# Optimization experiments

Measured on AMD Instinct MI355X. Metric: run time of the kernel, lower is better.

Reference implementation:

```python
import jax, jax.numpy as jnp
import numpy as np

SCORER_BIAS = 0.0
LN_EPS = 1e-5


def setup_inputs() -> dict:
    key = jax.random.key(0)
    k0, k1, k2 = jax.random.split(key, 3)
    B, L, D, H = 8, 8192, 1024, 256
    features = jax.random.normal(k0, (B, L, D), dtype=jnp.float32)
    gamma = jnp.ones((D,), jnp.float32)
    beta = jnp.zeros((D,), jnp.float32)
    W1 = (jax.random.normal(k1, (D, H)) * (1.0 / np.sqrt(D))).astype(jnp.float32)
    b1 = jnp.zeros((H,), jnp.float32)
    W2 = (jax.random.normal(k2, (H, 1)) * (1.0 / np.sqrt(H))).astype(jnp.float32)
    b2 = jnp.zeros((1,), jnp.float32)
    return {"features": features, "gamma": gamma, "beta": beta,
            "W1": W1, "b1": b1, "W2": W2, "b2": b2, "k": 512}


def reference(features, gamma, beta, W1, b1, W2, b2, k):
    # LayerNorm over last dim D
    mu = jnp.mean(features, axis=-1, keepdims=True)
    var = jnp.mean(jnp.square(features - mu), axis=-1, keepdims=True)
    x = (features - mu) * jax.lax.rsqrt(var + LN_EPS) * gamma + beta  # [B,L,D]
    # small MLP scorer: Linear -> GELU(exact, matches torch default) -> Linear
    h = jax.nn.gelu(jnp.einsum('bld,dh->blh', x, W1) + b1, approximate=False)
    scores = (jnp.einsum('blh,ho->blo', h, W2) + b2)[..., 0] + SCORER_BIAS  # [B,L]
    # per-row top-k (torch.topk semantics: largest, sorted)
    _, idx = jax.lax.top_k(scores, k)  # [B,k] int32
    # batched gather of original (un-normalized) features
    selected = jnp.take_along_axis(features, idx[..., None], axis=1)  # [B,k,D]
    return selected, scores, idx
```

## Files before the change

### kernel.cpp

```cpp
#include <hip/hip_runtime.h>
#include <math.h>

#define Dk 1024
#define Hk 256
#define Lk 8192
#define Bk 8
#define MTOT (Bk*Lk)

typedef _Float16 f16;
typedef __attribute__((ext_vector_type(8))) _Float16 f16x8;
typedef __attribute__((ext_vector_type(4))) float f32x4;
typedef unsigned long long u64;

#define AKG 520
#define ASP (8*AKG)
#define ABUF (2*ASP)

__global__ __launch_bounds__(1024) void prep_split(
    const float* __restrict__ W1, const float* __restrict__ gamma,
    const float* __restrict__ beta, f16* __restrict__ W1F,
    float* __restrict__ Spart, float* __restrict__ Tpart) {
  __shared__ float ps[1024], pt[1024];
  const int b = blockIdx.x, t = threadIdx.x;
  float sa = 0.f, ta = 0.f;
  #pragma unroll
  for (int j = 0; j < 4; ++j) {
    int idx = j * 65536 + b * 1024 + t;
    int d = idx >> 8, h = idx & 255;
    float w = W1[idx];
    float g = gamma[d];
    sa = fmaf(g, w, sa);
    ta = fmaf(beta[d], w, ta);
    float wg = g * w;
    f16 whi = (f16)wg;
    f16 wlp = (f16)((wg - (float)whi) * 2048.f);
    int ks = d >> 6, kg = (d >> 3) & 7, kk = d & 7;
    int nf = h >> 4, nn = h & 15;
    size_t base = ((((size_t)ks * 2) * 16 + nf) * 8 + kg) * 128 + nn * 8 + kk;
    W1F[base] = whi;
    W1F[base + 16384] = wlp;
  }
  ps[t] = sa; pt[t] = ta;
  __syncthreads();
  if (t < 256) {
    Spart[b * 256 + t] = ps[t] + ps[t + 256] + ps[t + 512] + ps[t + 768];
    Tpart[b * 256 + t] = pt[t] + pt[t + 256] + pt[t + 512] + pt[t + 768];
  }
}

__global__ __launch_bounds__(256) void prep_combine(
    const float* __restrict__ Spart, const float* __restrict__ Tpart,
    const float* __restrict__ b1, float* __restrict__ S, float* __restrict__ Tb) {
  int j = threadIdx.x;
  float s = 0.f, t = 0.f;
  for (int b = 0; b < 64; ++b) { s += Spart[b * 256 + j]; t += Tpart[b * 256 + j]; }
  S[j] = s;
  Tb[j] = t + b1[j];
}

#define MM3(aA, aB, ah, ax, wh, wl)                                            \
  aA = __builtin_amdgcn_mfma_f32_16x16x32_f16(ah, wh, aA, 0, 0, 0);            \
  aB = __builtin_amdgcn_mfma_f32_16x16x32_f16(ah, wl, aB, 0, 0, 0);            \
  aB = __builtin_amdgcn_mfma_f32_16x16x32_f16(ax, wh, aB, 0, 0, 0);

__global__ __launch_bounds__(512, 4) void scores_mfma(
    const float* __restrict__ F, const f16* __restrict__ W1F,
    const float* __restrict__ S, const float* __restrict__ Tb,
    const float* __restrict__ W2, const float* __restrict__ b2,
    float* __restrict__ scores_out) {
  __shared__ f16 As[2][ABUF];
  __shared__ float smu[64], srs[64];
  __shared__ float sred[64][4];

  const int tid = threadIdx.x;
  const int RM = blockIdx.x * 64;
  const int wid = tid >> 6, lane = tid & 63;
  const int wm = wid & 1, wn = wid >> 1;
  const int lg = lane >> 4, l15 = lane & 15;

  const int arow = tid >> 3, kg = tid & 7;
  const float* Aptr = F + (size_t)(RM + arow) * Dk + kg * 8;

  const int aoff0 = lg * AKG + (wm * 32 + l15) * 8;
  const int bwoff = (wn * 4) * 1024 + lg * 128 + l15 * 8;

  f32x4 accA[2][4], accB[2][4];
  #pragma unroll
  for (int i = 0; i < 2; ++i)
    #pragma unroll
    for (int j = 0; j < 4; ++j) {
      accA[i][j] = (f32x4){0.f, 0.f, 0.f, 0.f};
      accB[i][j] = (f32x4){0.f, 0.f, 0.f, 0.f};
    }

  float rsum = 0.f, rsq = 0.f;

#define SPLIT_STORE(buf, av0, av1)                                             \
  {                                                                            \
    f16x8 vhi, vlo;                                                            \
    _Pragma("unroll")                                                          \
    for (int e = 0; e < 8; ++e) {                                              \
      float x = (e < 4) ? ((e == 0) ? av0.x : (e == 1) ? av0.y                 \
                           : (e == 2) ? av0.z : av0.w)                         \
                        : ((e == 4) ? av1.x : (e == 5) ? av1.y                 \
                           : (e == 6) ? av1.z : av1.w);                        \
      rsum += x; rsq = fmaf(x, x, rsq);                                        \
      f16 hi = (f16)x;                                                         \
      vhi[e] = hi;                                                             \
      vlo[e] = (f16)((x - (float)hi) * 2048.f);                                \
    }                                                                          \
    *reinterpret_cast<f16x8*>(&As[buf][kg * AKG + arow * 8]) = vhi;            \
    *reinterpret_cast<f16x8*>(&As[buf][ASP + kg * AKG + arow * 8]) = vlo;      \
  }

  float4 av0 = *reinterpret_cast<const float4*>(Aptr);
  float4 av1 = *reinterpret_cast<const float4*>(Aptr + 4);
  SPLIT_STORE(0, av0, av1)
  av0 = *reinterpret_cast<const float4*>(Aptr + 64);
  av1 = *reinterpret_cast<const float4*>(Aptr + 68);
  __syncthreads();

  for (int s = 0; s < 16; ++s) {
    const int cur = s & 1;
    const f16* bs = W1F + (size_t)s * 32768 + bwoff;

    {
      f16x8 wh0 = *reinterpret_cast<const f16x8*>(bs);
      f16x8 wh1 = *reinterpret_cast<const f16x8*>(bs + 1024);
      f16x8 wl0 = *reinterpret_cast<const f16x8*>(bs + 16384);
      f16x8 wl1 = *reinterpret_cast<const f16x8*>(bs + 17408);
      const f16* ab = &As[cur][aoff0];
      f16x8 ahi0 = *reinterpret_cast<const f16x8*>(ab);
      f16x8 ahi1 = *reinterpret_cast<const f16x8*>(ab + 128);
      f16x8 axl0 = *reinterpret_cast<const f16x8*>(ab + ASP);
      f16x8 axl1 = *reinterpret_cast<const f16x8*>(ab + ASP + 128);
      if (s < 15) {
        SPLIT_STORE(cur ^ 1, av0, av1)
        if (s < 14) {
          av0 = *reinterpret_cast<const float4*>(Aptr + (s + 2) * 64);
          av1 = *reinterpret_cast<const float4*>(Aptr + (s + 2) * 64 + 4);
        }
      }
      MM3(accA[0][0], accB[0][0], ahi0, axl0, wh0, wl0)
      MM3(accA[1][0], accB[1][0], ahi1, axl1, wh0, wl0)
      MM3(accA[0][1], accB[0][1], ahi0, axl0, wh1, wl1)
      MM3(accA[1][1], accB[1][1], ahi1, axl1, wh1, wl1)
      wh0 = *reinterpret_cast<const f16x8*>(bs + 2048);
      wh1 = *reinterpret_cast<const f16x8*>(bs + 3072);
      wl0 = *reinterpret_cast<const f16x8*>(bs + 2048 + 16384);
      wl1 = *reinterpret_cast<const f16x8*>(bs + 3072 + 16384);
      MM3(accA[0][2], accB[0][2], ahi0, axl0, wh0, wl0)
      MM3(accA[1][2], accB[1][2], ahi1, axl1, wh0, wl0)
      MM3(accA[0][3], accB[0][3], ahi0, axl0, wh1, wl1)
      MM3(accA[1][3], accB[1][3], ahi1, axl1, wh1, wl1)
    }
    {
      f16x8 wh0 = *reinterpret_cast<const f16x8*>(bs + 512);
      f16x8 wh1 = *reinterpret_cast<const f16x8*>(bs + 512 + 1024);
      f16x8 wl0 = *reinterpret_cast<const f16x8*>(bs + 512 + 16384);
      f16x8 wl1 = *reinterpret_cast<const f16x8*>(bs + 512 + 17408);
      const f16* ab = &As[cur][aoff0 + 4 * AKG];
      f16x8 ahi0 = *reinterpret_cast<const f16x8*>(ab);
      f16x8 ahi1 = *reinterpret_cast<const f16x8*>(ab + 128);
      f16x8 axl0 = *reinterpret_cast<const f16x8*>(ab + ASP);
      f16x8 axl1 = *reinterpret_cast<const f16x8*>(ab + ASP + 128);
      MM3(accA[0][0], accB[0][0], ahi0, axl0, wh0, wl0)
      MM3(accA[1][0], accB[1][0], ahi1, axl1, wh0, wl0)
      MM3(accA[0][1], accB[0][1], ahi0, axl0, wh1, wl1)
      MM3(accA[1][1], accB[1][1], ahi1, axl1, wh1, wl1)
      wh0 = *reinterpret_cast<const f16x8*>(bs + 512 + 2048);
      wh1 = *reinterpret_cast<const f16x8*>(bs + 512 + 3072);
      wl0 = *reinterpret_cast<const f16x8*>(bs + 512 + 2048 + 16384);
      wl1 = *reinterpret_cast<const f16x8*>(bs + 512 + 3072 + 16384);
      MM3(accA[0][2], accB[0][2], ahi0, axl0, wh0, wl0)
      MM3(accA[1][2], accB[1][2], ahi1, axl1, wh0, wl0)
      MM3(accA[0][3], accB[0][3], ahi0, axl0, wh1, wl1)
      MM3(accA[1][3], accB[1][3], ahi1, axl1, wh1, wl1)
    }
    __syncthreads();
  }

  rsum += __shfl_xor(rsum, 1); rsum += __shfl_xor(rsum, 2); rsum += __shfl_xor(rsum, 4);
  rsq  += __shfl_xor(rsq, 1);  rsq  += __shfl_xor(rsq, 2);  rsq  += __shfl_xor(rsq, 4);
  if ((tid & 7) == 0) {
    float mu  = rsum * (1.f / 1024.f);
    float var = rsq * (1.f / 1024.f) - mu * mu;
    smu[arow] = mu;
    srs[arow] = rsqrtf(var + 1e-5f);
  }
  __syncthreads();

  float s2[4], tb2[4], w2v[4];
  #pragma unroll
  for (int nf = 0; nf < 4; ++nf) {
    int col = (wn * 4 + nf) * 16 + l15;
    s2[nf] = S[col]; tb2[nf] = Tb[col]; w2v[nf] = W2[col];
  }
  #pragma unroll
  for (int mf = 0; mf < 2; ++mf) {
    const int rbase = wm * 32 + mf * 16 + lg * 4;
    #pragma unroll
    for (int reg = 0; reg < 4; ++reg) {
      const int row = rbase + reg;
      float mu = smu[row], rs = srs[row];
      float part = 0.f;
      #pragma unroll
      for (int nf = 0; nf < 4; ++nf) {
        float val = accA[mf][nf][reg] + accB[mf][nf][reg] * (1.f / 2048.f);
        float hpre = rs * val - rs * mu * s2[nf] + tb2[nf];
        float g = 0.5f * hpre * (1.f + erff(hpre * 0.70710678118654752f));
        part = fmaf(g, w2v[nf], part);
      }
      part += __shfl_xor(part, 1); part += __shfl_xor(part, 2);
      part += __shfl_xor(part, 4); part += __shfl_xor(part, 8);
      if (l15 == 0) sred[row][wn] = part;
    }
  }
  __syncthreads();
  if (tid < 64) {
    float sc = b2[0] + sred[tid][0] + sred[tid][1] + sred[tid][2] + sred[tid][3];
    scores_out[RM + tid] = sc;
  }
}

__global__ __launch_bounds__(512) void topk_stage1(
    const float* __restrict__ scores, u64* __restrict__ kout) {
  __shared__ u64 keys[1024];
  const int blk = blockIdx.x;
  const int batch = blk >> 3, chunk = blk & 7;
  const int t = threadIdx.x;
  #pragma unroll
  for (int j = 0; j < 2; ++j) {
    int i = t + j * 512;
    int gi = chunk * 1024 + i;
    unsigned u = __float_as_uint(scores[(size_t)batch * Lk + gi]);
    unsigned mono = (u & 0x80000000u) ? ~u : (u | 0x80000000u);
    keys[i] = ((u64)(~mono) << 32) | (unsigned)gi;
  }
  __syncthreads();
  for (int size = 2; size <= 1024; size <<= 1) {
    for (int stride = size >> 1; stride > 0; stride >>= 1) {
      int lo = ((t & ~(stride - 1)) << 1) | (t & (stride - 1));
      int hi = lo + stride;
      bool up = ((lo & size) == 0);
      u64 a = keys[lo], c = keys[hi];
      if ((a > c) == up) { keys[lo] = c; keys[hi] = a; }
      __syncthreads();
    }
  }
  kout[(size_t)blk * 512 + t] = keys[t];
}

__global__ __launch_bounds__(512) void topk_stage2(
    const u64* __restrict__ kin, int k,
    float* __restrict__ idx_f, int* __restrict__ idx_i) {
  __shared__ u64 kk[4096];
  __shared__ u64 tmp[2048];
  const int b = blockIdx.x, t = threadIdx.x;
  #pragma unroll
  for (int j = 0; j < 8; ++j) kk[t + j * 512] = kin[(size_t)b * 4096 + t + j * 512];
  __syncthreads();
  #pragma unroll
  for (int j = 0; j < 4; ++j) {
    u64 a = kk[j * 1024 + t];
    u64 c = kk[j * 1024 + 512 + (511 - t)];
    tmp[j * 512 + t] = a < c ? a : c;
  }
  __syncthreads();
  for (int stride = 256; stride > 0; stride >>= 1) {
    #pragma unroll
    for (int w = 0; w < 2; ++w) {
      int p = t + w * 512;
      int r = p >> 8, q = p & 255;
      int lo = r * 512 + (((q & ~(stride - 1)) << 1) | (q & (stride - 1)));
      u64 a = tmp[lo], c = tmp[lo + stride];
      if (a > c) { tmp[lo] = c; tmp[lo + stride] = a; }
    }
    __syncthreads();
  }
  #pragma unroll
  for (int j = 0; j < 2; ++j) {
    u64 a = tmp[j * 1024 + t];
    u64 c = tmp[j * 1024 + 512 + (511 - t)];
    kk[j * 512 + t] = a < c ? a : c;
  }
  __syncthreads();
  for (int stride = 256; stride > 0; stride >>= 1) {
    int r = t >> 8, q = t & 255;
    int lo = r * 512 + (((q & ~(stride - 1)) << 1) | (q & (stride - 1)));
    u64 a = kk[lo], c = kk[lo + stride];
    if (a > c) { kk[lo] = c; kk[lo + stride] = a; }
    __syncthreads();
  }
  {
    u64 a = kk[t];
    u64 c = kk[512 + (511 - t)];
    tmp[t] = a < c ? a : c;
  }
  __syncthreads();
  for (int stride = 256; stride > 0; stride >>= 1) {
    if (t < 256) {
      int lo = ((t & ~(stride - 1)) << 1) | (t & (stride - 1));
      u64 a = tmp[lo], c = tmp[lo + stride];
      if (a > c) { tmp[lo] = c; tmp[lo + stride] = a; }
    }
    __syncthreads();
  }
  if (t < k) {
    int id = (int)(tmp[t] & 0xFFFFFFFFu);
    idx_f[(size_t)b * k + t] = (float)id;
    idx_i[(size_t)b * k + t] = id;
  }
}

__global__ __launch_bounds__(256) void gather_kernel(
    const float* __restrict__ F, const int* __restrict__ idx,
    float* __restrict__ out, int k) {
  int row = blockIdx.x;
  int b = row / k;
  int id = idx[row];
  const float4* src = reinterpret_cast<const float4*>(F + ((size_t)b * Lk + id) * Dk);
  float4* dst = reinterpret_cast<float4*>(out + (size_t)row * Dk);
  dst[threadIdx.x] = src[threadIdx.x];
}

extern "C" void kernel_launch(void* const* d_in, const int* in_sizes, int n_in,
                              void* d_out, int out_size, void* d_ws, size_t ws_size,
                              hipStream_t stream) {
  const float* F     = (const float*)d_in[0];
  const float* gamma = (const float*)d_in[1];
  const float* beta  = (const float*)d_in[2];
  const float* W1    = (const float*)d_in[3];
  const float* b1    = (const float*)d_in[4];
  const float* W2    = (const float*)d_in[5];
  const float* b2    = (const float*)d_in[6];
  int k = (out_size - Bk * Lk) / (Bk * Dk + Bk);

  float* out_sel = (float*)d_out;
  float* out_sc  = out_sel + (size_t)Bk * k * Dk;
  float* out_idx = out_sc + (size_t)Bk * Lk;

  f16*   W1F   = (f16*)d_ws;
  u64*   kout  = (u64*)((char*)d_ws + (1 << 20));
  float* Spart = (float*)((char*)kout + 262144);
  float* Tpart = Spart + 16384;
  float* Sp    = Tpart + 16384;
  float* Tbp   = Sp + Hk;
  int*   idxi  = (int*)(Tbp + Hk);

  hipLaunchKernelGGL(prep_split,   dim3(64),        dim3(1024), 0, stream,
                     W1, gamma, beta, W1F, Spart, Tpart);
  hipLaunchKernelGGL(prep_combine, dim3(1),         dim3(Hk),   0, stream,
                     Spart, Tpart, b1, Sp, Tbp);
  hipLaunchKernelGGL(scores_mfma,  dim3(MTOT / 64), dim3(512),  0, stream,
                     F, W1F, Sp, Tbp, W2, b2, out_sc);
  hipLaunchKernelGGL(topk_stage1,  dim3(64),        dim3(512),  0, stream,
                     out_sc, kout);
  hipLaunchKernelGGL(topk_stage2,  dim3(Bk),        dim3(512),  0, stream,
                     kout, k, out_idx, idxi);
  hipLaunchKernelGGL(gather_kernel, dim3(Bk * k),   dim3(256),  0, stream,
                     F, idxi, out_sel, k);
}
```

Measured before the change: 161.8 us.

## Stage W1 tiles in LDS via direct global-to-LDS loads with larger row tiles

The scores kernel now uses 128-row tiles with 1024 threads and a K step of 32 instead of 64. Each K step's split fp16 W1 tile is loaded once per block into double-buffered shared memory with global_load_lds, so warps no longer each read W1 from global or L2. W1F is repacked to match the new layout. The aim is to cut redundant weight traffic and improve reuse, at the cost of more barriers (32 steps), more LDS per block, and possibly lower occupancy.

```diff
diff --git a/kernel.cpp b/kernel.cpp
--- a/kernel.cpp
+++ b/kernel.cpp
@@ -9,12 +9,19 @@
 
 typedef _Float16 f16;
 typedef __attribute__((ext_vector_type(8))) _Float16 f16x8;
+typedef __attribute__((ext_vector_type(4))) _Float16 f16x4;
 typedef __attribute__((ext_vector_type(4))) float f32x4;
 typedef unsigned long long u64;
 
-#define AKG 520
-#define ASP (8*AKG)
+#define AROW 40
+#define ASP (128*AROW)
 #define ABUF (2*ASP)
+#define BSTEP 16384
+
+#define GLD_LDS16(g, l)                                                        \
+  __builtin_amdgcn_global_load_lds(                                            \
+      (const __attribute__((address_space(1))) unsigned int*)(g),              \
+      (__attribute__((address_space(3))) unsigned int*)(l), 16, 0, 0)
 
 __global__ __launch_bounds__(1024) void prep_split(
     const float* __restrict__ W1, const float* __restrict__ gamma,
@@ -34,11 +41,11 @@
     float wg = g * w;
     f16 whi = (f16)wg;
     f16 wlp = (f16)((wg - (float)whi) * 2048.f);
-    int ks = d >> 6, kg = (d >> 3) & 7, kk = d & 7;
+    int ks = d >> 5, kg = (d >> 3) & 3, kk = d & 7;
     int nf = h >> 4, nn = h & 15;
-    size_t base = ((((size_t)ks * 2) * 16 + nf) * 8 + kg) * 128 + nn * 8 + kk;
+    size_t base = (size_t)ks * BSTEP + (size_t)nf * 512 + kg * 128 + nn * 8 + kk;
     W1F[base] = whi;
-    W1F[base + 16384] = wlp;
+    W1F[base + 8192] = wlp;
   }
   ps[t] = sa; pt[t] = ta;
   __syncthreads();
@@ -63,119 +70,86 @@
   aB = __builtin_amdgcn_mfma_f32_16x16x32_f16(ah, wl, aB, 0, 0, 0);            \
   aB = __builtin_amdgcn_mfma_f32_16x16x32_f16(ax, wh, aB, 0, 0, 0);
 
-__global__ __launch_bounds__(512, 4) void scores_mfma(
+__global__ __launch_bounds__(1024) void scores_mfma(
     const float* __restrict__ F, const f16* __restrict__ W1F,
     const float* __restrict__ S, const float* __restrict__ Tb,
     const float* __restrict__ W2, const float* __restrict__ b2,
     float* __restrict__ scores_out) {
-  __shared__ f16 As[2][ABUF];
-  __shared__ float smu[64], srs[64];
-  __shared__ float sred[64][4];
+  __shared__ __align__(16) f16 As[2][ABUF];
+  __shared__ __align__(16) f16 Bs[2][BSTEP];
+  __shared__ float smu[128], srs[128];
+  __shared__ float sred[128][8];
 
   const int tid = threadIdx.x;
-  const int RM = blockIdx.x * 64;
+  const int RM = blockIdx.x * 128;
   const int wid = tid >> 6, lane = tid & 63;
   const int wm = wid & 1, wn = wid >> 1;
   const int lg = lane >> 4, l15 = lane & 15;
 
-  const int arow = tid >> 3, kg = tid & 7;
-  const float* Aptr = F + (size_t)(RM + arow) * Dk + kg * 8;
-
-  const int aoff0 = lg * AKG + (wm * 32 + l15) * 8;
-  const int bwoff = (wn * 4) * 1024 + lg * 128 + l15 * 8;
-
-  f32x4 accA[2][4], accB[2][4];
-  #pragma unroll
-  for (int i = 0; i < 2; ++i)
-    #pragma unroll
-    for (int j = 0; j < 4; ++j) {
+  const int arow = tid >> 3, sub = tid & 7;
+  const int awoff = arow * AROW + (sub >> 1) * 8 + (sub & 1) * 4;
+  const float* Aptr = F + (size_t)(RM + arow) * Dk + sub * 4;
+
+  const int aoff = (wm * 64 + l15) * AROW + lg * 8;
+  const int boff = (wn * 2) * 512 + lg * 128 + l15 * 8;
+
+  f32x4 accA[4][2], accB[4][2];
+  #pragma unroll
+  for (int i = 0; i < 4; ++i)
+    #pragma unroll
+    for (int j = 0; j < 2; ++j) {
       accA[i][j] = (f32x4){0.f, 0.f, 0.f, 0.f};
       accB[i][j] = (f32x4){0.f, 0.f, 0.f, 0.f};
     }
 
   float rsum = 0.f, rsq = 0.f;
 
-#define SPLIT_STORE(buf, av0, av1)                                             \
+#define SPLIT4(buf, fv)                                                        \
   {                                                                            \
-    f16x8 vhi, vlo;                                                            \
+    f16x4 vhi, vlo;                                                            \
     _Pragma("unroll")                                                          \
-    for (int e = 0; e < 8; ++e) {                                              \
-      float x = (e < 4) ? ((e == 0) ? av0.x : (e == 1) ? av0.y                 \
-                           : (e == 2) ? av0.z : av0.w)                         \
-                        : ((e == 4) ? av1.x : (e == 5) ? av1.y                 \
-                           : (e == 6) ? av1.z : av1.w);                        \
+    for (int e = 0; e < 4; ++e) {                                              \
+      float x = (e == 0) ? fv.x : (e == 1) ? fv.y : (e == 2) ? fv.z : fv.w;    \
       rsum += x; rsq = fmaf(x, x, rsq);                                        \
       f16 hi = (f16)x;                                                         \
       vhi[e] = hi;                                                             \
       vlo[e] = (f16)((x - (float)hi) * 2048.f);                                \
     }                                                                          \
-    *reinterpret_cast<f16x8*>(&As[buf][kg * AKG + arow * 8]) = vhi;            \
-    *reinterpret_cast<f16x8*>(&As[buf][ASP + kg * AKG + arow * 8]) = vlo;      \
-  }
-
-  float4 av0 = *reinterpret_cast<const float4*>(Aptr);
-  float4 av1 = *reinterpret_cast<const float4*>(Aptr + 4);
-  SPLIT_STORE(0, av0, av1)
-  av0 = *reinterpret_cast<const float4*>(Aptr + 64);
-  av1 = *reinterpret_cast<const float4*>(Aptr + 68);
-  __syncthreads();
-
-  for (int s = 0; s < 16; ++s) {
+    *reinterpret_cast<f16x4*>(&As[buf][awoff])       = vhi;                    \
+    *reinterpret_cast<f16x4*>(&As[buf][ASP + awoff]) = vlo;                    \
+  }
+
+#define STAGE_B(buf, step)                                                     \
+  {                                                                            \
+    const f16* bsrc = W1F + (size_t)(step) * BSTEP;                            \
+    GLD_LDS16(bsrc + (size_t)tid * 8, &Bs[buf][tid * 8]);                      \
+    GLD_LDS16(bsrc + (size_t)(1024 + tid) * 8, &Bs[buf][(1024 + tid) * 8]);    \
+  }
+
+  STAGE_B(0, 0)
+  float4 av = *reinterpret_cast<const float4*>(Aptr);
+  SPLIT4(0, av)
+  av = *reinterpret_cast<const float4*>(Aptr + 32);
+  __syncthreads();
+
+  for (int s = 0; s < 32; ++s) {
     const int cur = s & 1;
-    const f16* bs = W1F + (size_t)s * 32768 + bwoff;
-
-    {
-      f16x8 wh0 = *reinterpret_cast<const f16x8*>(bs);
-      f16x8 wh1 = *reinterpret_cast<const f16x8*>(bs + 1024);
-      f16x8 wl0 = *reinterpret_cast<const f16x8*>(bs + 16384);
-      f16x8 wl1 = *reinterpret_cast<const f16x8*>(bs + 17408);
-      const f16* ab = &As[cur][aoff0];
-      f16x8 ahi0 = *reinterpret_cast<const f16x8*>(ab);
-      f16x8 ahi1 = *reinterpret_cast<const f16x8*>(ab + 128);
-      f16x8 axl0 = *reinterpret_cast<const f16x8*>(ab + ASP);
-      f16x8 axl1 = *reinterpret_cast<const f16x8*>(ab + ASP + 128);
-      if (s < 15) {
-        SPLIT_STORE(cur ^ 1, av0, av1)
-        if (s < 14) {
-          av0 = *reinterpret_cast<const float4*>(Aptr + (s + 2) * 64);
-          av1 = *reinterpret_cast<const float4*>(Aptr + (s + 2) * 64 + 4);
-        }
-      }
-      MM3(accA[0][0], accB[0][0], ahi0, axl0, wh0, wl0)
-      MM3(accA[1][0], accB[1][0], ahi1, axl1, wh0, wl0)
-      MM3(accA[0][1], accB[0][1], ahi0, axl0, wh1, wl1)
-      MM3(accA[1][1], accB[1][1], ahi1, axl1, wh1, wl1)
-      wh0 = *reinterpret_cast<const f16x8*>(bs + 2048);
-      wh1 = *reinterpret_cast<const f16x8*>(bs + 3072);
-      wl0 = *reinterpret_cast<const f16x8*>(bs + 2048 + 16384);
-      wl1 = *reinterpret_cast<const f16x8*>(bs + 3072 + 16384);
-      MM3(accA[0][2], accB[0][2], ahi0, axl0, wh0, wl0)
-      MM3(accA[1][2], accB[1][2], ahi1, axl1, wh0, wl0)
-      MM3(accA[0][3], accB[0][3], ahi0, axl0, wh1, wl1)
-      MM3(accA[1][3], accB[1][3], ahi1, axl1, wh1, wl1)
-    }
-    {
-      f16x8 wh0 = *reinterpret_cast<const f16x8*>(bs + 512);
-      f16x8 wh1 = *reinterpret_cast<const f16x8*>(bs + 512 + 1024);
-      f16x8 wl0 = *reinterpret_cast<const f16x8*>(bs + 512 + 16384);
-      f16x8 wl1 = *reinterpret_cast<const f16x8*>(bs + 512 + 17408);
-      const f16* ab = &As[cur][aoff0 + 4 * AKG];
-      f16x8 ahi0 = *reinterpret_cast<const f16x8*>(ab);
-      f16x8 ahi1 = *reinterpret_cast<const f16x8*>(ab + 128);
-      f16x8 axl0 = *reinterpret_cast<const f16x8*>(ab + ASP);
-      f16x8 axl1 = *reinterpret_cast<const f16x8*>(ab + ASP + 128);
-      MM3(accA[0][0], accB[0][0], ahi0, axl0, wh0, wl0)
-      MM3(accA[1][0], accB[1][0], ahi1, axl1, wh0, wl0)
-      MM3(accA[0][1], accB[0][1], ahi0, axl0, wh1, wl1)
-      MM3(accA[1][1], accB[1][1], ahi1, axl1, wh1, wl1)
-      wh0 = *reinterpret_cast<const f16x8*>(bs + 512 + 2048);
-      wh1 = *reinterpret_cast<const f16x8*>(bs + 512 + 3072);
-      wl0 = *reinterpret_cast<const f16x8*>(bs + 512 + 2048 + 16384);
-      wl1 = *reinterpret_cast<const f16x8*>(bs + 512 + 3072 + 16384);
-      MM3(accA[0][2], accB[0][2], ahi0, axl0, wh0, wl0)
-      MM3(accA[1][2], accB[1][2], ahi1, axl1, wh0, wl0)
-      MM3(accA[0][3], accB[0][3], ahi0, axl0, wh1, wl1)
-      MM3(accA[1][3], accB[1][3], ahi1, axl1, wh1, wl1)
+    if (s < 31) {
+      STAGE_B(cur ^ 1, s + 1)
+      SPLIT4(cur ^ 1, av)
+      if (s < 30) av = *reinterpret_cast<const float4*>(Aptr + (s + 2) * 32);
+    }
+    f16x8 wh0 = *reinterpret_cast<const f16x8*>(&Bs[cur][boff]);
+    f16x8 wl0 = *reinterpret_cast<const f16x8*>(&Bs[cur][boff + 8192]);
+    f16x8 wh1 = *reinterpret_cast<const f16x8*>(&Bs[cur][boff + 512]);
+    f16x8 wl1 = *reinterpret_cast<const f16x8*>(&Bs[cur][boff + 512 + 8192]);
+    #pragma unroll
+    for (int mf = 0; mf < 4; ++mf) {
+      const int ao = aoff + mf * (16 * AROW);
+      f16x8 ahi = *reinterpret_cast<const f16x8*>(&As[cur][ao]);
+      f16x8 axl = *reinterpret_cast<const f16x8*>(&As[cur][ASP + ao]);
+      MM3(accA[mf][0], accB[mf][0], ahi, axl, wh0, wl0)
+      MM3(accA[mf][1], accB[mf][1], ahi, axl, wh1, wl1)
     }
     __syncthreads();
   }
@@ -190,22 +164,22 @@
   }
   __syncthreads();
 
-  float s2[4], tb2[4], w2v[4];
-  #pragma unroll
-  for (int nf = 0; nf < 4; ++nf) {
-    int col = (wn * 4 + nf) * 16 + l15;
+  float s2[2], tb2[2], w2v[2];
+  #pragma unroll
+  for (int nf = 0; nf < 2; ++nf) {
+    int col = wn * 32 + nf * 16 + l15;
     s2[nf] = S[col]; tb2[nf] = Tb[col]; w2v[nf] = W2[col];
   }
   #pragma unroll
-  for (int mf = 0; mf < 2; ++mf) {
-    const int rbase = wm * 32 + mf * 16 + lg * 4;
+  for (int mf = 0; mf < 4; ++mf) {
+    const int rbase = wm * 64 + mf * 16 + lg * 4;
     #pragma unroll
     for (int reg = 0; reg < 4; ++reg) {
       const int row = rbase + reg;
       float mu = smu[row], rs = srs[row];
       float part = 0.f;
       #pragma unroll
-      for (int nf = 0; nf < 4; ++nf) {
+      for (int nf = 0; nf < 2; ++nf) {
         float val = accA[mf][nf][reg] + accB[mf][nf][reg] * (1.f / 2048.f);
         float hpre = rs * val - rs * mu * s2[nf] + tb2[nf];
         float g = 0.5f * hpre * (1.f + erff(hpre * 0.70710678118654752f));
@@ -217,8 +191,10 @@
     }
   }
   __syncthreads();
-  if (tid < 64) {
-    float sc = b2[0] + sred[tid][0] + sred[tid][1] + sred[tid][2] + sred[tid][3];
+  if (tid < 128) {
+    float sc = b2[0];
+    #pragma unroll
+    for (int w = 0; w < 8; ++w) sc += sred[tid][w];
     scores_out[RM + tid] = sc;
   }
 }
@@ -348,16 +324,16 @@
   float* Tbp   = Sp + Hk;
   int*   idxi  = (int*)(Tbp + Hk);
 
-  hipLaunchKernelGGL(prep_split,   dim3(64),        dim3(1024), 0, stream,
+  hipLaunchKernelGGL(prep_split,   dim3(64),         dim3(1024), 0, stream,
                      W1, gamma, beta, W1F, Spart, Tpart);
-  hipLaunchKernelGGL(prep_combine, dim3(1),         dim3(Hk),   0, stream,
+  hipLaunchKernelGGL(prep_combine, dim3(1),          dim3(Hk),   0, stream,
                      Spart, Tpart, b1, Sp, Tbp);
-  hipLaunchKernelGGL(scores_mfma,  dim3(MTOT / 64), dim3(512),  0, stream,
+  hipLaunchKernelGGL(scores_mfma,  dim3(MTOT / 128), dim3(1024), 0, stream,
                      F, W1F, Sp, Tbp, W2, b2, out_sc);
-  hipLaunchKernelGGL(topk_stage1,  dim3(64),        dim3(512),  0, stream,
+  hipLaunchKernelGGL(topk_stage1,  dim3(64),         dim3(512),  0, stream,
                      out_sc, kout);
-  hipLaunchKernelGGL(topk_stage2,  dim3(Bk),        dim3(512),  0, stream,
+  hipLaunchKernelGGL(topk_stage2,  dim3(Bk),         dim3(512),  0, stream,
                      kout, k, out_idx, idxi);
-  hipLaunchKernelGGL(gather_kernel, dim3(Bk * k),   dim3(256),  0, stream,
+  hipLaunchKernelGGL(gather_kernel, dim3(Bk * k),    dim3(256),  0, stream,
                      F, idxi, out_sel, k);
 }
```

Result: slower. 196.6 us (+21.5%).

## Retile scores GEMM to 128-row blocks with 16 waves each owning 16 columns

Applied to the files above, without the earlier changes.

The scores kernel now processes 128 rows per block with 1024 threads, and each of the 16 waves owns one 16-column slice of H across all 128 rows instead of a 32x64 sub-tile. Each W1 fragment is loaded from global once per wave per k-step and reused across 8 row fragments, which cuts redundant weight traffic per row. LDS grows (AKG doubled), occupancy hints are dropped, and the final reduction runs over 16 partials per row. Every A fragment is now read from LDS by all 16 waves, which raises LDS read pressure, and fewer resident waves per CU may hurt latency hiding.

```diff
diff --git a/kernel.cpp b/kernel.cpp
--- a/kernel.cpp
+++ b/kernel.cpp
@@ -12,7 +12,7 @@
 typedef __attribute__((ext_vector_type(4))) float f32x4;
 typedef unsigned long long u64;
 
-#define AKG 520
+#define AKG 1048
 #define ASP (8*AKG)
 #define ABUF (2*ASP)
 
@@ -63,35 +63,32 @@
   aB = __builtin_amdgcn_mfma_f32_16x16x32_f16(ah, wl, aB, 0, 0, 0);            \
   aB = __builtin_amdgcn_mfma_f32_16x16x32_f16(ax, wh, aB, 0, 0, 0);
 
-__global__ __launch_bounds__(512, 4) void scores_mfma(
+__global__ __launch_bounds__(1024) void scores_mfma(
     const float* __restrict__ F, const f16* __restrict__ W1F,
     const float* __restrict__ S, const float* __restrict__ Tb,
     const float* __restrict__ W2, const float* __restrict__ b2,
     float* __restrict__ scores_out) {
-  __shared__ f16 As[2][ABUF];
-  __shared__ float smu[64], srs[64];
-  __shared__ float sred[64][4];
+  __shared__ __align__(16) f16 As[2][ABUF];
+  __shared__ float smu[128], srs[128];
+  __shared__ float sred[128][16];
 
   const int tid = threadIdx.x;
-  const int RM = blockIdx.x * 64;
+  const int RM = blockIdx.x * 128;
   const int wid = tid >> 6, lane = tid & 63;
-  const int wm = wid & 1, wn = wid >> 1;
   const int lg = lane >> 4, l15 = lane & 15;
 
   const int arow = tid >> 3, kg = tid & 7;
   const float* Aptr = F + (size_t)(RM + arow) * Dk + kg * 8;
 
-  const int aoff0 = lg * AKG + (wm * 32 + l15) * 8;
-  const int bwoff = (wn * 4) * 1024 + lg * 128 + l15 * 8;
-
-  f32x4 accA[2][4], accB[2][4];
-  #pragma unroll
-  for (int i = 0; i < 2; ++i)
-    #pragma unroll
-    for (int j = 0; j < 4; ++j) {
-      accA[i][j] = (f32x4){0.f, 0.f, 0.f, 0.f};
-      accB[i][j] = (f32x4){0.f, 0.f, 0.f, 0.f};
-    }
+  const int aoff = lg * AKG + l15 * 8;
+  const int boff = wid * 1024 + lg * 128 + l15 * 8;
+
+  f32x4 accA[8], accB[8];
+  #pragma unroll
+  for (int i = 0; i < 8; ++i) {
+    accA[i] = (f32x4){0.f, 0.f, 0.f, 0.f};
+    accB[i] = (f32x4){0.f, 0.f, 0.f, 0.f};
+  }
 
   float rsum = 0.f, rsq = 0.f;
 
@@ -122,60 +119,31 @@
 
   for (int s = 0; s < 16; ++s) {
     const int cur = s & 1;
-    const f16* bs = W1F + (size_t)s * 32768 + bwoff;
-
-    {
-      f16x8 wh0 = *reinterpret_cast<const f16x8*>(bs);
-      f16x8 wh1 = *reinterpret_cast<const f16x8*>(bs + 1024);
-      f16x8 wl0 = *reinterpret_cast<const f16x8*>(bs + 16384);
-      f16x8 wl1 = *reinterpret_cast<const f16x8*>(bs + 17408);
-      const f16* ab = &As[cur][aoff0];
-      f16x8 ahi0 = *reinterpret_cast<const f16x8*>(ab);
-      f16x8 ahi1 = *reinterpret_cast<const f16x8*>(ab + 128);
-      f16x8 axl0 = *reinterpret_cast<const f16x8*>(ab + ASP);
-      f16x8 axl1 = *reinterpret_cast<const f16x8*>(ab + ASP + 128);
-      if (s < 15) {
-        SPLIT_STORE(cur ^ 1, av0, av1)
-        if (s < 14) {
-          av0 = *reinterpret_cast<const float4*>(Aptr + (s + 2) * 64);
-          av1 = *reinterpret_cast<const float4*>(Aptr + (s + 2) * 64 + 4);
-        }
+    const f16* bs = W1F + (size_t)s * 32768 + boff;
+    f16x8 wh0 = *reinterpret_cast<const f16x8*>(bs);
+    f16x8 wl0 = *reinterpret_cast<const f16x8*>(bs + 16384);
+    f16x8 wh1 = *reinterpret_cast<const f16x8*>(bs + 512);
+    f16x8 wl1 = *reinterpret_cast<const f16x8*>(bs + 512 + 16384);
+    if (s < 15) {
+      SPLIT_STORE(cur ^ 1, av0, av1)
+      if (s < 14) {
+        av0 = *reinterpret_cast<const float4*>(Aptr + (s + 2) * 64);
+        av1 = *reinterpret_cast<const float4*>(Aptr + (s + 2) * 64 + 4);
       }
-      MM3(accA[0][0], accB[0][0], ahi0, axl0, wh0, wl0)
-      MM3(accA[1][0], accB[1][0], ahi1, axl1, wh0, wl0)
-      MM3(accA[0][1], accB[0][1], ahi0, axl0, wh1, wl1)
-      MM3(accA[1][1], accB[1][1], ahi1, axl1, wh1, wl1)
-      wh0 = *reinterpret_cast<const f16x8*>(bs + 2048);
-      wh1 = *reinterpret_cast<const f16x8*>(bs + 3072);
-      wl0 = *reinterpret_cast<const f16x8*>(bs + 2048 + 16384);
-      wl1 = *reinterpret_cast<const f16x8*>(bs + 3072 + 16384);
-      MM3(accA[0][2], accB[0][2], ahi0, axl0, wh0, wl0)
-      MM3(accA[1][2], accB[1][2], ahi1, axl1, wh0, wl0)
-      MM3(accA[0][3], accB[0][3], ahi0, axl0, wh1, wl1)
-      MM3(accA[1][3], accB[1][3], ahi1, axl1, wh1, wl1)
-    }
-    {
-      f16x8 wh0 = *reinterpret_cast<const f16x8*>(bs + 512);
-      f16x8 wh1 = *reinterpret_cast<const f16x8*>(bs + 512 + 1024);
-      f16x8 wl0 = *reinterpret_cast<const f16x8*>(bs + 512 + 16384);
-      f16x8 wl1 = *reinterpret_cast<const f16x8*>(bs + 512 + 17408);
-      const f16* ab = &As[cur][aoff0 + 4 * AKG];
-      f16x8 ahi0 = *reinterpret_cast<const f16x8*>(ab);
-      f16x8 ahi1 = *reinterpret_cast<const f16x8*>(ab + 128);
-      f16x8 axl0 = *reinterpret_cast<const f16x8*>(ab + ASP);
-      f16x8 axl1 = *reinterpret_cast<const f16x8*>(ab + ASP + 128);
-      MM3(accA[0][0], accB[0][0], ahi0, axl0, wh0, wl0)
-      MM3(accA[1][0], accB[1][0], ahi1, axl1, wh0, wl0)
-      MM3(accA[0][1], accB[0][1], ahi0, axl0, wh1, wl1)
-      MM3(accA[1][1], accB[1][1], ahi1, axl1, wh1, wl1)
-      wh0 = *reinterpret_cast<const f16x8*>(bs + 512 + 2048);
-      wh1 = *reinterpret_cast<const f16x8*>(bs + 512 + 3072);
-      wl0 = *reinterpret_cast<const f16x8*>(bs + 512 + 2048 + 16384);
-      wl1 = *reinterpret_cast<const f16x8*>(bs + 512 + 3072 + 16384);
-      MM3(accA[0][2], accB[0][2], ahi0, axl0, wh0, wl0)
-      MM3(accA[1][2], accB[1][2], ahi1, axl1, wh0, wl0)
-      MM3(accA[0][3], accB[0][3], ahi0, axl0, wh1, wl1)
-      MM3(accA[1][3], accB[1][3], ahi1, axl1, wh1, wl1)
+    }
+    #pragma unroll
+    for (int mf = 0; mf < 8; ++mf) {
+      const int ao = aoff + mf * 128;
+      f16x8 ahi = *reinterpret_cast<const f16x8*>(&As[cur][ao]);
+      f16x8 axl = *reinterpret_cast<const f16x8*>(&As[cur][ASP + ao]);
+      MM3(accA[mf], accB[mf], ahi, axl, wh0, wl0)
+    }
+    #pragma unroll
+    for (int mf = 0; mf < 8; ++mf) {
+      const int ao = aoff + 4 * AKG + mf * 128;
+      f16x8 ahi = *reinterpret_cast<const f16x8*>(&As[cur][ao]);
+      f16x8 axl = *reinterpret_cast<const f16x8*>(&As[cur][ASP + ao]);
+      MM3(accA[mf], accB[mf], ahi, axl, wh1, wl1)
     }
     __syncthreads();
   }
@@ -190,35 +158,29 @@
   }
   __syncthreads();
 
-  float s2[4], tb2[4], w2v[4];
-  #pragma unroll
-  for (int nf = 0; nf < 4; ++nf) {
-    int col = (wn * 4 + nf) * 16 + l15;
-    s2[nf] = S[col]; tb2[nf] = Tb[col]; w2v[nf] = W2[col];
-  }
-  #pragma unroll
-  for (int mf = 0; mf < 2; ++mf) {
-    const int rbase = wm * 32 + mf * 16 + lg * 4;
+  const int col = wid * 16 + l15;
+  const float s2 = S[col], tb2 = Tb[col], w2v = W2[col];
+  #pragma unroll
+  for (int mf = 0; mf < 8; ++mf) {
+    const int rbase = mf * 16 + lg * 4;
     #pragma unroll
     for (int reg = 0; reg < 4; ++reg) {
       const int row = rbase + reg;
       float mu = smu[row], rs = srs[row];
-      float part = 0.f;
-      #pragma unroll
-      for (int nf = 0; nf < 4; ++nf) {
-        float val = accA[mf][nf][reg] + accB[mf][nf][reg] * (1.f / 2048.f);
-        float hpre = rs * val - rs * mu * s2[nf] + tb2[nf];
-        float g = 0.5f * hpre * (1.f + erff(hpre * 0.70710678118654752f));
-        part = fmaf(g, w2v[nf], part);
-      }
+      float val = accA[mf][reg] + accB[mf][reg] * (1.f / 2048.f);
+      float hpre = rs * val - rs * mu * s2 + tb2;
+      float g = 0.5f * hpre * (1.f + erff(hpre * 0.70710678118654752f));
+      float part = g * w2v;
       part += __shfl_xor(part, 1); part += __shfl_xor(part, 2);
       part += __shfl_xor(part, 4); part += __shfl_xor(part, 8);
-      if (l15 == 0) sred[row][wn] = part;
-    }
-  }
-  __syncthreads();
-  if (tid < 64) {
-    float sc = b2[0] + sred[tid][0] + sred[tid][1] + sred[tid][2] + sred[tid][3];
+      if (l15 == 0) sred[row][wid] = part;
+    }
+  }
+  __syncthreads();
+  if (tid < 128) {
+    float sc = b2[0];
+    #pragma unroll
+    for (int w = 0; w < 16; ++w) sc += sred[tid][w];
     scores_out[RM + tid] = sc;
   }
 }
@@ -348,16 +310,16 @@
   float* Tbp   = Sp + Hk;
   int*   idxi  = (int*)(Tbp + Hk);
 
-  hipLaunchKernelGGL(prep_split,   dim3(64),        dim3(1024), 0, stream,
+  hipLaunchKernelGGL(prep_split,   dim3(64),         dim3(1024), 0, stream,
                      W1, gamma, beta, W1F, Spart, Tpart);
-  hipLaunchKernelGGL(prep_combine, dim3(1),         dim3(Hk),   0, stream,
+  hipLaunchKernelGGL(prep_combine, dim3(1),          dim3(Hk),   0, stream,
                      Spart, Tpart, b1, Sp, Tbp);
-  hipLaunchKernelGGL(scores_mfma,  dim3(MTOT / 64), dim3(512),  0, stream,
+  hipLaunchKernelGGL(scores_mfma,  dim3(MTOT / 128), dim3(1024), 0, stream,
                      F, W1F, Sp, Tbp, W2, b2, out_sc);
-  hipLaunchKernelGGL(topk_stage1,  dim3(64),        dim3(512),  0, stream,
+  hipLaunchKernelGGL(topk_stage1,  dim3(64),         dim3(512),  0, stream,
                      out_sc, kout);
-  hipLaunchKernelGGL(topk_stage2,  dim3(Bk),        dim3(512),  0, stream,
+  hipLaunchKernelGGL(topk_stage2,  dim3(Bk),         dim3(512),  0, stream,
                      kout, k, out_idx, idxi);
-  hipLaunchKernelGGL(gather_kernel, dim3(Bk * k),   dim3(256),  0, stream,
+  hipLaunchKernelGGL(gather_kernel, dim3(Bk * k),    dim3(256),  0, stream,
                      F, idxi, out_sel, k);
 }
```

Result: faster. 156.7 us (median of 2 runs) (-3.2%).
